# Performance work log

Measured on AMD Instinct MI355X. Metric: run time of the kernel, lower is better.

Reference implementation:

```python
import jax, jax.numpy as jnp
import numpy as np

N = 100000   # nodes
E = 500000   # edges
H = 128      # h_dim
TAU = 1.0    # gumbel-softmax temperature (module default)


def setup_inputs() -> dict:
    key = jax.random.key(0)
    k = jax.random.split(key, 6)
    h = jax.random.normal(k[0], (N, H), dtype=jnp.float32)
    W1 = jax.random.normal(k[1], (2 * H, H // 2), dtype=jnp.float32) / np.float32(np.sqrt(2 * H))
    b1 = jnp.zeros((H // 2,), dtype=jnp.float32)
    W2 = jax.random.normal(k[2], (H // 2, 1), dtype=jnp.float32) / np.float32(np.sqrt(H // 2))
    b2 = jnp.zeros((1,), dtype=jnp.float32)
    u = jax.random.uniform(k[3], (E, 2), dtype=jnp.float32, minval=1e-6, maxval=1.0)
    edge_index = jax.random.randint(k[4], (2, E), 0, N, dtype=jnp.int32)
    return {"h": h, "W1": W1, "b1": b1, "W2": W2, "b2": b2, "u": u, "edge_index": edge_index}


def reference(h, W1, b1, W2, b2, u, edge_index):
    row, col = edge_index[0], edge_index[1]
    # gather endpoint features and concat: [E, 2H]
    edge_feat = jnp.concatenate([h[row], h[col]], axis=-1)
    # 2-layer MLP scorer -> per-edge logit [E]
    hid = jax.nn.relu(edge_feat @ W1 + b1)
    logits = (hid @ W2 + b2)[:, 0]
    # binary gumbel-softmax over [keep-logit=0, logit]
    samp_logits = jnp.stack([jnp.zeros_like(logits), logits], axis=-1)  # [E, 2]
    g = -jnp.log(-jnp.log(u))  # gumbel noise from uniform
    y_soft = jax.nn.softmax((samp_logits + g) / TAU, axis=-1)
    # hard=True straight-through
    idx = jnp.argmax(y_soft, axis=-1)
    y_hard = jax.nn.one_hot(idx, 2, dtype=y_soft.dtype)
    y = y_hard - jax.lax.stop_gradient(y_soft) + y_soft
    weights = y[:, 1]
    return (weights, logits)
```

## Files before the change

### kernel.cpp

```cpp
#include <hip/hip_runtime.h>
#include <math.h>

#define NN 100000
#define NE 500000

__global__ __launch_bounds__(256)
void node_proj(const float* __restrict__ h, const float* __restrict__ W1,
               const float* __restrict__ b1, float* __restrict__ AB, int nnodes)
{
    __shared__ float lh[64 * 132];

    const int t  = threadIdx.x;
    const int g  = blockIdx.x >> 1;
    const int jh = blockIdx.x & 1;
    const int n0 = g * 64;

#pragma unroll
    for (int i = 0; i < 8; ++i) {
        int flat = i * 256 + t;
        int nl = flat >> 5;
        int c  = flat & 31;
        int ng = n0 + nl;
        float4 v = make_float4(0.f, 0.f, 0.f, 0.f);
        if (ng < nnodes) v = *(const float4*)&h[(size_t)ng * 128 + c * 4];
        *(float4*)&lh[nl * 132 + c * 4] = v;
    }
    __syncthreads();

    const int wid  = __builtin_amdgcn_readfirstlane(t >> 6);
    const int lane = t & 63;
    const int jq   = jh * 64 + wid * 16;

    const float* Wbase = (jq < 64) ? (W1 + jq) : (W1 + 128 * 64 + (jq - 64));

    float acc[16];
#pragma unroll
    for (int i = 0; i < 16; ++i) acc[i] = (jq < 64) ? b1[jq + i] : 0.f;

    const int lbase = lane * 132;

#pragma unroll 2
    for (int k4 = 0; k4 < 32; ++k4) {
        float4 hv = *(const float4*)&lh[lbase + k4 * 4];
#pragma unroll
        for (int kk = 0; kk < 4; ++kk) {
            const float* wr = Wbase + (k4 * 4 + kk) * 64;
            float hk = (kk == 0) ? hv.x : (kk == 1) ? hv.y
                     : (kk == 2) ? hv.z : hv.w;
#pragma unroll
            for (int q = 0; q < 4; ++q) {
                float4 w4 = *(const float4*)&wr[q * 4];
                acc[q * 4 + 0] += hk * w4.x;
                acc[q * 4 + 1] += hk * w4.y;
                acc[q * 4 + 2] += hk * w4.z;
                acc[q * 4 + 3] += hk * w4.w;
            }
        }
    }

    const int n = n0 + lane;
    if (n < nnodes) {
        float* orow = AB + (size_t)n * 128 + jq;
#pragma unroll
        for (int q = 0; q < 4; ++q)
            *(float4*)&orow[q * 4] = make_float4(acc[q * 4 + 0], acc[q * 4 + 1],
                                                 acc[q * 4 + 2], acc[q * 4 + 3]);
    }
}

__global__ __launch_bounds__(256)
void edge_sample(const float* __restrict__ AB, const float* __restrict__ W2,
                 const float* __restrict__ b2, const float* __restrict__ u,
                 const int* __restrict__ ei, float* __restrict__ out)
{
    int t = threadIdx.x;
    int l = t & 15;
    int e = blockIdx.x * 16 + (t >> 4);

    int row = ei[e];
    int col = ei[NE + e];

    float4 a = *(const float4*)&AB[(size_t)row * 128 + l * 4];
    float4 b = *(const float4*)&AB[(size_t)col * 128 + 64 + l * 4];
    float4 w = *(const float4*)&W2[l * 4];

    float h0 = fmaxf(a.x + b.x, 0.f);
    float h1 = fmaxf(a.y + b.y, 0.f);
    float h2 = fmaxf(a.z + b.z, 0.f);
    float h3 = fmaxf(a.w + b.w, 0.f);

    float p = h0 * w.x + h1 * w.y + h2 * w.z + h3 * w.w;
    p += __shfl_xor(p, 1);
    p += __shfl_xor(p, 2);
    p += __shfl_xor(p, 4);
    p += __shfl_xor(p, 8);

    if (l == 0) {
        float logit = p + b2[0];
        float u0 = u[2 * e];
        float u1 = u[2 * e + 1];
        float g0 = -logf(-logf(u0));
        float g1 = -logf(-logf(u1));
        out[e]      = (logit + g1 > g0) ? 1.0f : 0.0f;
        out[NE + e] = logit;
    }
}

__global__ __launch_bounds__(256)
void edge_direct(const float* __restrict__ h, const float* __restrict__ W1,
                 const float* __restrict__ b1, const float* __restrict__ W2,
                 const float* __restrict__ b2, const float* __restrict__ u,
                 const int* __restrict__ ei, float* __restrict__ out)
{
    int t = threadIdx.x;
    int l = t & 15;
    int e = blockIdx.x * 16 + (t >> 4);

    int row = ei[e];
    int col = ei[NE + e];

    float a0 = 0.f, a1 = 0.f, a2 = 0.f, a3 = 0.f;
    const float* hr = h + (size_t)row * 128;
    const float* hc = h + (size_t)col * 128;

    for (int k4 = 0; k4 < 32; ++k4) {
        float4 hv = *(const float4*)&hr[k4 * 4];
#pragma unroll
        for (int kk = 0; kk < 4; ++kk) {
            float4 wr = *(const float4*)&W1[(k4 * 4 + kk) * 64 + l * 4];
            float hval = (&hv.x)[kk];
            a0 += hval * wr.x; a1 += hval * wr.y; a2 += hval * wr.z; a3 += hval * wr.w;
        }
    }
    for (int k4 = 0; k4 < 32; ++k4) {
        float4 hv = *(const float4*)&hc[k4 * 4];
#pragma unroll
        for (int kk = 0; kk < 4; ++kk) {
            float4 wr = *(const float4*)&W1[(128 + k4 * 4 + kk) * 64 + l * 4];
            float hval = (&hv.x)[kk];
            a0 += hval * wr.x; a1 += hval * wr.y; a2 += hval * wr.z; a3 += hval * wr.w;
        }
    }
    float4 bb = *(const float4*)&b1[l * 4];
    float4 w  = *(const float4*)&W2[l * 4];
    float h0 = fmaxf(a0 + bb.x, 0.f);
    float h1 = fmaxf(a1 + bb.y, 0.f);
    float h2 = fmaxf(a2 + bb.z, 0.f);
    float h3 = fmaxf(a3 + bb.w, 0.f);

    float p = h0 * w.x + h1 * w.y + h2 * w.z + h3 * w.w;
    p += __shfl_xor(p, 1);
    p += __shfl_xor(p, 2);
    p += __shfl_xor(p, 4);
    p += __shfl_xor(p, 8);

    if (l == 0) {
        float logit = p + b2[0];
        float u0 = u[2 * e];
        float u1 = u[2 * e + 1];
        float g0 = -logf(-logf(u0));
        float g1 = -logf(-logf(u1));
        out[e]      = (logit + g1 > g0) ? 1.0f : 0.0f;
        out[NE + e] = logit;
    }
}

extern "C" void kernel_launch(void* const* d_in, const int* in_sizes, int n_in,
                              void* d_out, int out_size, void* d_ws, size_t ws_size,
                              hipStream_t stream)
{
    const float* h  = (const float*)d_in[0];
    const float* W1 = (const float*)d_in[1];
    const float* b1 = (const float*)d_in[2];
    const float* W2 = (const float*)d_in[3];
    const float* b2 = (const float*)d_in[4];
    const float* u  = (const float*)d_in[5];
    const int*   ei = (const int*)d_in[6];
    float* out = (float*)d_out;

    const size_t need = (size_t)NN * 128 * sizeof(float);
    if (ws_size >= need) {
        float* AB = (float*)d_ws;
        int ngroups = (NN + 63) / 64;
        node_proj<<<ngroups * 2, 256, 0, stream>>>(h, W1, b1, AB, NN);
        edge_sample<<<NE / 16, 256, 0, stream>>>(AB, W2, b2, u, ei, out);
    } else {
        edge_direct<<<NE / 16, 256, 0, stream>>>(h, W1, b1, W2, b2, u, ei, out);
    }
}
```

Measured before the change: 111.2 us.

## Register-tile node projection as 8 nodes by 8 outputs per thread

The node projection kernel now has each block handle 128 nodes and compute both W1 halves, so each h row is staged into LDS once instead of twice. Each thread accumulates an 8-node by 8-output register tile. It double-buffers its W1 slices in registers across k-steps so the next weights load while the current ones are used. The LDS row stride becomes 133 floats to spread banks, which leaves the float4 LDS accesses misaligned. The much larger LDS footprint and register count also lower occupancy, trading it against higher arithmetic reuse.

```diff
diff --git a/kernel.cpp b/kernel.cpp
--- a/kernel.cpp
+++ b/kernel.cpp
@@ -8,63 +8,98 @@
 void node_proj(const float* __restrict__ h, const float* __restrict__ W1,
                const float* __restrict__ b1, float* __restrict__ AB, int nnodes)
 {
-    __shared__ float lh[64 * 132];
-
-    const int t  = threadIdx.x;
-    const int g  = blockIdx.x >> 1;
-    const int jh = blockIdx.x & 1;
-    const int n0 = g * 64;
-
-#pragma unroll
-    for (int i = 0; i < 8; ++i) {
+    __shared__ float lh[128 * 133];
+
+    const int t   = threadIdx.x;
+    const int tj  = t & 15;
+    const int tnf = t >> 4;
+    const int n0  = blockIdx.x * 128;
+
+#pragma unroll
+    for (int i = 0; i < 16; ++i) {
         int flat = i * 256 + t;
         int nl = flat >> 5;
         int c  = flat & 31;
         int ng = n0 + nl;
         float4 v = make_float4(0.f, 0.f, 0.f, 0.f);
         if (ng < nnodes) v = *(const float4*)&h[(size_t)ng * 128 + c * 4];
-        *(float4*)&lh[nl * 132 + c * 4] = v;
+        *(float4*)&lh[nl * 133 + c * 4] = v;
     }
     __syncthreads();
 
-    const int wid  = __builtin_amdgcn_readfirstlane(t >> 6);
-    const int lane = t & 63;
-    const int jq   = jh * 64 + wid * 16;
-
-    const float* Wbase = (jq < 64) ? (W1 + jq) : (W1 + 128 * 64 + (jq - 64));
-
-    float acc[16];
-#pragma unroll
-    for (int i = 0; i < 16; ++i) acc[i] = (jq < 64) ? b1[jq + i] : 0.f;
-
-    const int lbase = lane * 132;
-
-#pragma unroll 2
-    for (int k4 = 0; k4 < 32; ++k4) {
-        float4 hv = *(const float4*)&lh[lbase + k4 * 4];
-#pragma unroll
-        for (int kk = 0; kk < 4; ++kk) {
-            const float* wr = Wbase + (k4 * 4 + kk) * 64;
-            float hk = (kk == 0) ? hv.x : (kk == 1) ? hv.y
-                     : (kk == 2) ? hv.z : hv.w;
-#pragma unroll
-            for (int q = 0; q < 4; ++q) {
-                float4 w4 = *(const float4*)&wr[q * 4];
-                acc[q * 4 + 0] += hk * w4.x;
-                acc[q * 4 + 1] += hk * w4.y;
-                acc[q * 4 + 2] += hk * w4.z;
-                acc[q * 4 + 3] += hk * w4.w;
-            }
+    const float* wa_base = W1 + tj * 4;
+    const float* wb_base = W1 + 128 * 64 + tj * 4;
+
+    float acc[8][8];
+    {
+        float4 bv = *(const float4*)&b1[tj * 4];
+#pragma unroll
+        for (int r = 0; r < 8; ++r) {
+            acc[r][0] = bv.x; acc[r][1] = bv.y; acc[r][2] = bv.z; acc[r][3] = bv.w;
+            acc[r][4] = 0.f;  acc[r][5] = 0.f;  acc[r][6] = 0.f;  acc[r][7] = 0.f;
         }
     }
 
-    const int n = n0 + lane;
-    if (n < nnodes) {
-        float* orow = AB + (size_t)n * 128 + jq;
-#pragma unroll
-        for (int q = 0; q < 4; ++q)
-            *(float4*)&orow[q * 4] = make_float4(acc[q * 4 + 0], acc[q * 4 + 1],
-                                                 acc[q * 4 + 2], acc[q * 4 + 3]);
+    float4 A0[4], B0[4], A1[4], B1[4];
+#pragma unroll
+    for (int kk = 0; kk < 4; ++kk) {
+        A0[kk] = *(const float4*)&wa_base[kk * 64];
+        B0[kk] = *(const float4*)&wb_base[kk * 64];
+    }
+
+#define LOAD_W(AX, BX, K4)                                              \
+    _Pragma("unroll")                                                   \
+    for (int kk = 0; kk < 4; ++kk) {                                    \
+        AX[kk] = *(const float4*)&wa_base[((K4) * 4 + kk) * 64];        \
+        BX[kk] = *(const float4*)&wb_base[((K4) * 4 + kk) * 64];        \
+    }
+
+#define COMPUTE(AX, BX, K4)                                             \
+    {                                                                   \
+        float4 hv[8];                                                   \
+        _Pragma("unroll")                                               \
+        for (int r = 0; r < 8; ++r)                                     \
+            hv[r] = *(const float4*)&lh[(tnf + 16 * r) * 133 + (K4) * 4]; \
+        _Pragma("unroll")                                               \
+        for (int kk = 0; kk < 4; ++kk) {                                \
+            float4 wa = AX[kk], wb = BX[kk];                            \
+            _Pragma("unroll")                                           \
+            for (int r = 0; r < 8; ++r) {                               \
+                float hk = (kk == 0) ? hv[r].x : (kk == 1) ? hv[r].y    \
+                         : (kk == 2) ? hv[r].z : hv[r].w;               \
+                acc[r][0] += hk * wa.x;                                 \
+                acc[r][1] += hk * wa.y;                                 \
+                acc[r][2] += hk * wa.z;                                 \
+                acc[r][3] += hk * wa.w;                                 \
+                acc[r][4] += hk * wb.x;                                 \
+                acc[r][5] += hk * wb.y;                                 \
+                acc[r][6] += hk * wb.z;                                 \
+                acc[r][7] += hk * wb.w;                                 \
+            }                                                           \
+        }                                                               \
+    }
+
+#pragma unroll 1
+    for (int k4 = 0; k4 < 30; k4 += 2) {
+        LOAD_W(A1, B1, k4 + 1)
+        COMPUTE(A0, B0, k4)
+        LOAD_W(A0, B0, k4 + 2)
+        COMPUTE(A1, B1, k4 + 1)
+    }
+    LOAD_W(A1, B1, 31)
+    COMPUTE(A0, B0, 30)
+    COMPUTE(A1, B1, 31)
+
+#undef LOAD_W
+#undef COMPUTE
+
+#pragma unroll
+    for (int r = 0; r < 8; ++r) {
+        int ng = n0 + tnf + 16 * r;
+        if (ng >= nnodes) continue;
+        float* orow = AB + (size_t)ng * 128;
+        *(float4*)&orow[tj * 4]      = make_float4(acc[r][0], acc[r][1], acc[r][2], acc[r][3]);
+        *(float4*)&orow[64 + tj * 4] = make_float4(acc[r][4], acc[r][5], acc[r][6], acc[r][7]);
     }
 }
 
@@ -181,8 +216,8 @@
     const size_t need = (size_t)NN * 128 * sizeof(float);
     if (ws_size >= need) {
         float* AB = (float*)d_ws;
-        int ngroups = (NN + 63) / 64;
-        node_proj<<<ngroups * 2, 256, 0, stream>>>(h, W1, b1, AB, NN);
+        int nblocks = (NN + 127) / 128;
+        node_proj<<<nblocks, 256, 0, stream>>>(h, W1, b1, AB, NN);
         edge_sample<<<NE / 16, 256, 0, stream>>>(AB, W2, b2, u, ei, out);
     } else {
         edge_direct<<<NE / 16, 256, 0, stream>>>(h, W1, b1, W2, b2, u, ei, out);
```

New measurement: 98.04 us. 1.13x faster.
